# Optimization experiments

Hardware: AMD Instinct MI355X
Metric: run time of the kernel (lower is better)

Reference implementation:

```python
import jax, jax.numpy as jnp
import numpy as np

N, E, IC, H, OC, K = 100000, 1600000, 64, 64, 16, 4
BN_EPS = 1e-5


def setup_inputs() -> dict:
    key = jax.random.key(0)
    ks = jax.random.split(key, 32)
    s = 0.05
    inp = {
        'x': jax.random.normal(ks[0], (N, IC), jnp.float32),
        'edge_index': jax.random.randint(ks[1], (2, E), 0, N, jnp.int32),
        # ChebConv weights: K linear maps (no bias) + one bias per conv (PyG ChebConv)
        'W1': jax.random.normal(ks[2], (K, IC, H), jnp.float32) * s,
        'bc1': jax.random.normal(ks[3], (H,), jnp.float32) * s,
        'W2': jax.random.normal(ks[4], (K, H, H), jnp.float32) * s,
        'bc2': jax.random.normal(ks[5], (H,), jnp.float32) * s,
        'W3': jax.random.normal(ks[6], (K, H, H), jnp.float32) * s,
        'bc3': jax.random.normal(ks[7], (H,), jnp.float32) * s,
        # BatchNorm1d params + running stats (eval mode)
        'g1': 1.0 + 0.1 * jax.random.normal(ks[8], (H,), jnp.float32),
        'be1': 0.1 * jax.random.normal(ks[9], (H,), jnp.float32),
        'rm1': 0.1 * jax.random.normal(ks[10], (H,), jnp.float32),
        'rv1': jax.random.uniform(ks[11], (H,), jnp.float32, 0.5, 1.5),
        'g2': 1.0 + 0.1 * jax.random.normal(ks[12], (H,), jnp.float32),
        'be2': 0.1 * jax.random.normal(ks[13], (H,), jnp.float32),
        'rm2': 0.1 * jax.random.normal(ks[14], (H,), jnp.float32),
        'rv2': jax.random.uniform(ks[15], (H,), jnp.float32, 0.5, 1.5),
        'g3': 1.0 + 0.1 * jax.random.normal(ks[16], (H,), jnp.float32),
        'be3': 0.1 * jax.random.normal(ks[17], (H,), jnp.float32),
        'rm3': 0.1 * jax.random.normal(ks[18], (H,), jnp.float32),
        'rv3': jax.random.uniform(ks[19], (H,), jnp.float32, 0.5, 1.5),
        # head Linear(h, oc)
        'headW': jax.random.normal(ks[20], (H, OC), jnp.float32) * s,
        'headB': jax.random.normal(ks[21], (OC,), jnp.float32) * s,
    }
    return inp


def _prop(x, src, dst, w):
    # one sparse propagation: out[dst] += w_e * x[src]  (== L_hat @ x)
    return jax.ops.segment_sum(w[:, None] * x[src], dst, num_segments=N)


def _cheb(x, src, dst, w, W, b):
    # Chebyshev recursion: T0 = x, T1 = L_hat x, T_k = 2 L_hat T_{k-1} - T_{k-2}
    Tx0 = x
    out = Tx0 @ W[0]
    Tx1 = _prop(x, src, dst, w)
    out = out + Tx1 @ W[1]
    for k in range(2, W.shape[0]):
        Tx2 = 2.0 * _prop(Tx1, src, dst, w) - Tx0
        out = out + Tx2 @ W[k]
        Tx0, Tx1 = Tx1, Tx2
    return out + b


def _bn(x, g, b, rm, rv):
    # BatchNorm1d in eval mode: affine with running stats
    return (x - rm) * (g * jax.lax.rsqrt(rv + BN_EPS)) + b


def reference(x, edge_index, W1, bc1, W2, bc2, W3, bc3,
              g1, be1, rm1, rv1, g2, be2, rm2, rv2, g3, be3, rm3, rv3,
              headW, headB):
    src, dst = edge_index[0], edge_index[1]
    # sym-normalized scaled Laplacian (lambda_max=2): L_hat = -D^{-1/2} A D^{-1/2}
    deg = jax.ops.segment_sum(jnp.ones((E,), x.dtype), src, num_segments=N)
    dinv = jnp.where(deg > 0, jax.lax.rsqrt(jnp.maximum(deg, 1.0)), 0.0)
    w = -dinv[src] * dinv[dst]
    h = jax.nn.relu(_bn(_cheb(x, src, dst, w, W1, bc1), g1, be1, rm1, rv1))
    h = jax.nn.relu(_bn(_cheb(h, src, dst, w, W2, bc2), g2, be2, rm2, rv2))
    h = jax.nn.relu(_bn(_cheb(h, src, dst, w, W3, bc3), g3, be3, rm3, rv3))
    return h @ headW + headB
```

## Files before the change

### kernel.cpp

```cpp
#include <hip/hip_runtime.h>

#define NN 100000
#define EE 1600000
#define HD 64
#define OCD 16
#define NBUCK 391
#define CAP 5888
#define BN_EPS 1e-5f

typedef unsigned short u16;
typedef unsigned long long u64;
typedef __attribute__((ext_vector_type(8))) short short8v;
typedef __attribute__((ext_vector_type(4))) float f32x4;

union f32u32 { float f; unsigned int u; };

__device__ __forceinline__ float bflo(unsigned int u) {
    f32u32 c; c.u = u << 16; return c.f;
}
__device__ __forceinline__ float bfhi(unsigned int u) {
    f32u32 c; c.u = u & 0xffff0000u; return c.f;
}
__device__ __forceinline__ float bf2f(u16 u) {
    f32u32 c; c.u = (unsigned int)u << 16; return c.f;
}
__device__ __forceinline__ u16 f2bf(float f) {
    f32u32 c; c.f = f;
    unsigned int r = 0x7fffu + ((c.u >> 16) & 1u);
    return (u16)((c.u + r) >> 16);
}

__global__ __launch_bounds__(256) void bucketA_kernel(
        const int* __restrict__ src, const int* __restrict__ dst,
        int* __restrict__ gcd, u64* __restrict__ bregion) {
    __shared__ int lh[NBUCK], lbase[NBUCK], lcur[NBUCK];
    int t = threadIdx.x;
    int ebase = blockIdx.x * 4096;

    for (int i = t; i < NBUCK; i += 256) lh[i] = 0;
    __syncthreads();

    int es[16], ed[16];
    #pragma unroll
    for (int j = 0; j < 16; ++j) {
        int e = ebase + j * 256 + t;
        if (e < EE) {
            es[j] = src[e]; ed[j] = dst[e];
            atomicAdd(&lh[ed[j] >> 8], 1);
        } else { es[j] = -1; ed[j] = 0; }
    }
    __syncthreads();
    for (int i = t; i < NBUCK; i += 256) {
        int c = lh[i];
        lbase[i] = (c > 0) ? atomicAdd(&gcd[i * 16], c) : 0;
        lcur[i] = 0;
    }
    __syncthreads();
    #pragma unroll
    for (int j = 0; j < 16; ++j) {
        if (es[j] >= 0) {
            int b = ed[j] >> 8;
            int r = atomicAdd(&lcur[b], 1);
            int pos = lbase[b] + r;
            if (pos < CAP)
                bregion[(size_t)b * CAP + pos] =
                    (u64)(unsigned int)es[j] | ((u64)(unsigned int)ed[j] << 32);
        }
    }
}

__global__ __launch_bounds__(256) void bucketA2_kernel(
        const int* __restrict__ src,
        int* __restrict__ gcs, int* __restrict__ sregion) {
    __shared__ int lh[NBUCK], lbase[NBUCK], lcur[NBUCK];
    int t = threadIdx.x;
    int ebase = blockIdx.x * 4096;

    for (int i = t; i < NBUCK; i += 256) lh[i] = 0;
    __syncthreads();

    int es[16];
    #pragma unroll
    for (int j = 0; j < 16; ++j) {
        int e = ebase + j * 256 + t;
        if (e < EE) {
            es[j] = src[e];
            atomicAdd(&lh[es[j] >> 8], 1);
        } else es[j] = -1;
    }
    __syncthreads();
    for (int i = t; i < NBUCK; i += 256) {
        int c = lh[i];
        lbase[i] = (c > 0) ? atomicAdd(&gcs[i * 16], c) : 0;
        lcur[i] = 0;
    }
    __syncthreads();
    #pragma unroll
    for (int j = 0; j < 16; ++j) {
        if (es[j] >= 0) {
            int b = es[j] >> 8;
            int r = atomicAdd(&lcur[b], 1);
            int pos = lbase[b] + r;
            if (pos < CAP)
                sregion[(size_t)b * CAP + pos] = es[j];
        }
    }
}

__global__ __launch_bounds__(256) void bucketB_kernel(
        const int* __restrict__ gcd, const u64* __restrict__ bregion,
        int* __restrict__ rstart, int* __restrict__ deg,
        int* __restrict__ colp) {
    __shared__ int lh[256], lsc[256], lcur[256];
    int b = blockIdx.x, t = threadIdx.x;
    int cnt = min(gcd[b * 16], CAP - 768);
    size_t base = (size_t)b * CAP;

    lh[t] = 0;
    __syncthreads();
    for (int i = t; i < cnt; i += 256) {
        int d = (int)(bregion[base + i] >> 32);
        atomicAdd(&lh[d & 255], 1);
    }
    __syncthreads();
    int deg4 = (lh[t] + 3) & ~3;
    lsc[t] = deg4;
    __syncthreads();
    for (int o = 1; o < 256; o <<= 1) {
        int v = (t >= o) ? lsc[t - o] : 0;
        __syncthreads();
        lsc[t] += v;
        __syncthreads();
    }
    int excl = lsc[t] - deg4;
    int node = b * 256 + t;
    if (node < NN) {
        rstart[node] = (int)base + excl;
        deg[node] = lh[t];
    }
    lcur[t] = excl;
    __syncthreads();
    for (int i = t; i < cnt; i += 256) {
        u64 pair = bregion[base + i];
        int s = (int)(unsigned int)(pair & 0xffffffffu);
        int dl = ((int)(pair >> 32)) & 255;
        int p = atomicAdd(&lcur[dl], 1);
        colp[base + p] = s;
    }
}

__global__ __launch_bounds__(256) void bucketB2_kernel(
        const int* __restrict__ gcs, const int* __restrict__ sregion,
        int* __restrict__ cs) {
    __shared__ int lh[256];
    int b = blockIdx.x, t = threadIdx.x;
    int cnt = min(gcs[b * 16], CAP);
    size_t base = (size_t)b * CAP;

    lh[t] = 0;
    __syncthreads();
    for (int i = t; i < cnt; i += 256)
        atomicAdd(&lh[sregion[base + i] & 255], 1);
    __syncthreads();
    int node = b * 256 + t;
    if (node < NN) cs[node] = lh[t];
}

__global__ void dinv_kernel(const int* __restrict__ cs, float* __restrict__ dinv,
                            float* __restrict__ ndsq, float* __restrict__ sdeg) {
    int i = blockIdx.x * 256 + threadIdx.x;
    if (i < NN) {
        int d = cs[i];
        float di = (d > 0) ? rsqrtf((float)d) : 0.0f;
        dinv[i] = di;
        ndsq[i] = -di * di;
        sdeg[i] = (d > 0) ? sqrtf((float)d) : 0.0f;
    }
}

__global__ void fold_kernel(const float* __restrict__ W, const float* __restrict__ bc,
                            const float* __restrict__ g, const float* __restrict__ be,
                            const float* __restrict__ rm, const float* __restrict__ rv,
                            u16* __restrict__ Wfrag, float* __restrict__ biasf) {
    int idx = blockIdx.x * 256 + threadIdx.x;
    if (idx >= 16384) return;
    int km = idx >> 12, r = idx & 4095, i = r >> 6, h = r & 63;
    float sc = g[h] * rsqrtf(rv[h] + BN_EPS);
    int e = i * 64 + h;
    float wv;
    if      (km == 0) wv = (W[e] - W[8192 + e]) * sc;
    else if (km == 1) wv = (W[4096 + e] - 3.0f * W[12288 + e]) * sc;
    else if (km == 2) wv = 2.0f * W[8192 + e] * sc;
    else              wv = 4.0f * W[12288 + e] * sc;
    u16 hi = f2bf(wv);
    u16 lo = f2bf(wv - bf2f(hi));
    int lane = (((i & 31) >> 3) << 4) | (h & 15);
    int base = (km * 2) * 4096 + (i >> 5) * 2048 + (h >> 4) * 512 + lane * 8 + (i & 7);
    Wfrag[base] = hi;
    Wfrag[base + 4096] = lo;
    if (idx < 64)
        biasf[idx] = (bc[idx] - rm[idx]) * g[idx] * rsqrtf(rv[idx] + BN_EPS) + be[idx];
}

__global__ void scale0_kernel(const float* __restrict__ x, const float* __restrict__ dinv,
                              u16* __restrict__ Xhi, u16* __restrict__ Xlo,
                              u16* __restrict__ P0) {
    int idx = blockIdx.x * 256 + threadIdx.x;
    if (idx >= NN * (HD / 4)) return;
    int n = idx >> 4;
    float di = dinv[n];
    float4 v = ((const float4*)x)[idx];
    float vv[4] = {v.x, v.y, v.z, v.w};
    u16 hi[4], lo[4], p[4];
    #pragma unroll
    for (int j = 0; j < 4; ++j) {
        hi[j] = f2bf(vv[j]);
        lo[j] = f2bf(vv[j] - bf2f(hi[j]));
        p[j]  = f2bf(di * vv[j]);
    }
    *(u64*)(&Xhi[(size_t)idx * 4]) = *(u64*)hi;
    *(u64*)(&Xlo[(size_t)idx * 4]) = *(u64*)lo;
    *(u64*)(&P0 [(size_t)idx * 4]) = *(u64*)p;
}

__global__ __launch_bounds__(256) void prop_kernel(
        const u16* __restrict__ Pin, u16* __restrict__ Pout,
        const int* __restrict__ rstart, const int* __restrict__ deg,
        const int* __restrict__ col, const float* __restrict__ ndsq) {
    int d = blockIdx.x * 4 + (threadIdx.x >> 6);
    if (d >= NN) return;
    int lane = threadIdx.x & 63;
    int g = lane >> 4;
    int l = lane & 15;
    int e0 = rstart[d], e1 = e0 + deg[d];

    float a0 = 0.f, a1 = 0.f, a2 = 0.f, a3 = 0.f;
    for (int c = e0 + g * 4; c < e1; c += 16) {
        if (c + 4 <= e1) {
            int4 c4 = *(const int4*)(col + c);
            uint2 u0 = *(const uint2*)(Pin + (size_t)c4.x * HD + l * 4);
            uint2 u1 = *(const uint2*)(Pin + (size_t)c4.y * HD + l * 4);
            uint2 u2 = *(const uint2*)(Pin + (size_t)c4.z * HD + l * 4);
            uint2 u3 = *(const uint2*)(Pin + (size_t)c4.w * HD + l * 4);
            a0 += bflo(u0.x); a1 += bfhi(u0.x); a2 += bflo(u0.y); a3 += bfhi(u0.y);
            a0 += bflo(u1.x); a1 += bfhi(u1.x); a2 += bflo(u1.y); a3 += bfhi(u1.y);
            a0 += bflo(u2.x); a1 += bfhi(u2.x); a2 += bflo(u2.y); a3 += bfhi(u2.y);
            a0 += bflo(u3.x); a1 += bfhi(u3.x); a2 += bflo(u3.y); a3 += bfhi(u3.y);
        } else {
            for (int j = 0; j < e1 - c; ++j) {
                int s = col[c + j];
                uint2 u = *(const uint2*)(Pin + (size_t)s * HD + l * 4);
                a0 += bflo(u.x); a1 += bfhi(u.x);
                a2 += bflo(u.y); a3 += bfhi(u.y);
            }
        }
    }
    a0 += __shfl_xor(a0, 16); a1 += __shfl_xor(a1, 16);
    a2 += __shfl_xor(a2, 16); a3 += __shfl_xor(a3, 16);
    a0 += __shfl_xor(a0, 32); a1 += __shfl_xor(a1, 32);
    a2 += __shfl_xor(a2, 32); a3 += __shfl_xor(a3, 32);

    if (g == 0) {
        float nd = ndsq[d];
        uint2 o;
        o.x = (unsigned int)f2bf(nd * a0) | ((unsigned int)f2bf(nd * a1) << 16);
        o.y = (unsigned int)f2bf(nd * a2) | ((unsigned int)f2bf(nd * a3) << 16);
        *(uint2*)(Pout + (size_t)d * HD + l * 4) = o;
    }
}

template<bool FUSE_HEAD>
__global__ __launch_bounds__(256) void combine_kernel(
        const u16* __restrict__ Xhi, const u16* __restrict__ Xlo,
        const u16* __restrict__ P1, const u16* __restrict__ P2,
        const u16* __restrict__ P3,
        const float* __restrict__ sdeg, const float* __restrict__ dinv,
        const u16* __restrict__ Wfrag, const float* __restrict__ biasf,
        u16* __restrict__ outDhi, u16* __restrict__ outDlo, u16* __restrict__ outP0,
        const float* __restrict__ headW, const float* __restrict__ headB,
        float* __restrict__ out16) {
    int t = threadIdx.x;
    int w = t >> 6;
    int l = t & 63;
    int nbase = blockIdx.x * 64;

    int arow = nbase + w * 16 + (l & 15);
    if (arow > NN - 1) arow = NN - 1;
    size_t abase = (size_t)arow * HD;

    f32x4 accX[4], accP[4];
    #pragma unroll
    for (int nt = 0; nt < 4; ++nt) {
        accX[nt] = (f32x4){0.f, 0.f, 0.f, 0.f};
        accP[nt] = (f32x4){0.f, 0.f, 0.f, 0.f};
    }

    #pragma unroll
    for (int ks = 0; ks < 2; ++ks) {
        size_t ao = abase + ks * 32 + (l >> 4) * 8;
        short8v aXhi = *(const short8v*)(Xhi + ao);
        short8v aXlo = *(const short8v*)(Xlo + ao);
        short8v aP1  = *(const short8v*)(P1  + ao);
        short8v aP2  = *(const short8v*)(P2  + ao);
        short8v aP3  = *(const short8v*)(P3  + ao);
        #pragma unroll
        for (int nt = 0; nt < 4; ++nt) {
            const u16* wb = Wfrag + ks * 2048 + nt * 512 + l * 8;
            short8v b0h = *(const short8v*)(wb);
            short8v b0l = *(const short8v*)(wb + 4096);
            short8v b1h = *(const short8v*)(wb + 8192);
            short8v b1l = *(const short8v*)(wb + 12288);
            short8v b2h = *(const short8v*)(wb + 16384);
            short8v b2l = *(const short8v*)(wb + 20480);
            short8v b3h = *(const short8v*)(wb + 24576);
            short8v b3l = *(const short8v*)(wb + 28672);
            accX[nt] = __builtin_amdgcn_mfma_f32_16x16x32_bf16(aXhi, b0h, accX[nt], 0, 0, 0);
            accX[nt] = __builtin_amdgcn_mfma_f32_16x16x32_bf16(aXlo, b0h, accX[nt], 0, 0, 0);
            accX[nt] = __builtin_amdgcn_mfma_f32_16x16x32_bf16(aXhi, b0l, accX[nt], 0, 0, 0);
            accP[nt] = __builtin_amdgcn_mfma_f32_16x16x32_bf16(aP1,  b1h, accP[nt], 0, 0, 0);
            accP[nt] = __builtin_amdgcn_mfma_f32_16x16x32_bf16(aP1,  b1l, accP[nt], 0, 0, 0);
            accP[nt] = __builtin_amdgcn_mfma_f32_16x16x32_bf16(aP2,  b2h, accP[nt], 0, 0, 0);
            accP[nt] = __builtin_amdgcn_mfma_f32_16x16x32_bf16(aP2,  b2l, accP[nt], 0, 0, 0);
            accP[nt] = __builtin_amdgcn_mfma_f32_16x16x32_bf16(aP3,  b3h, accP[nt], 0, 0, 0);
            accP[nt] = __builtin_amdgcn_mfma_f32_16x16x32_bf16(aP3,  b3l, accP[nt], 0, 0, 0);
        }
    }

    int col = l & 15;
    int rbase = w * 16 + (l >> 4) * 4;

    if (!FUSE_HEAD) {
        #pragma unroll
        for (int nt = 0; nt < 4; ++nt) {
            int h = nt * 16 + col;
            float bi = biasf[h];
            #pragma unroll
            for (int reg = 0; reg < 4; ++reg) {
                int node = nbase + rbase + reg;
                int nodeL = node > NN - 1 ? NN - 1 : node;
                float val = accX[nt][reg] + sdeg[nodeL] * accP[nt][reg] + bi;
                val = fmaxf(val, 0.f);
                if (node < NN) {
                    u16 hi = f2bf(val);
                    size_t o = (size_t)node * HD + h;
                    outDhi[o] = hi;
                    outDlo[o] = f2bf(val - bf2f(hi));
                    outP0[o]  = f2bf(dinv[nodeL] * val);
                }
            }
        }
    } else {
        __shared__ float Tl[64][68];
        __shared__ float Wl[HD * OCD];
        #pragma unroll
        for (int nt = 0; nt < 4; ++nt) {
            int h = nt * 16 + col;
            float bi = biasf[h];
            #pragma unroll
            for (int reg = 0; reg < 4; ++reg) {
                int node = nbase + rbase + reg;
                int nodeL = node > NN - 1 ? NN - 1 : node;
                float val = accX[nt][reg] + sdeg[nodeL] * accP[nt][reg] + bi;
                Tl[rbase + reg][h] = fmaxf(val, 0.f);
            }
        }
        ((float4*)Wl)[t & 255] = ((const float4*)headW)[t & 255];
        __syncthreads();

        int n = t >> 2;
        int oc0 = (t & 3) * 4;
        float4 o;
        o.x = headB[oc0]; o.y = headB[oc0 + 1]; o.z = headB[oc0 + 2]; o.w = headB[oc0 + 3];
        #pragma unroll 8
        for (int i = 0; i < 64; ++i) {
            float tv = Tl[n][i];
            const float* wr = &Wl[i * OCD + oc0];
            o.x = fmaf(tv, wr[0], o.x);
            o.y = fmaf(tv, wr[1], o.y);
            o.z = fmaf(tv, wr[2], o.z);
            o.w = fmaf(tv, wr[3], o.w);
        }
        int nn = nbase + n;
        if (nn < NN) *(float4*)(&out16[(size_t)nn * OCD + oc0]) = o;
    }
}

static inline size_t al256(size_t x) { return (x + 255) & ~(size_t)255; }

extern "C" void kernel_launch(void* const* d_in, const int* in_sizes, int n_in,
                              void* d_out, int out_size, void* d_ws, size_t ws_size,
                              hipStream_t stream) {
    const float* x     = (const float*)d_in[0];
    const int*   ei    = (const int*)  d_in[1];
    const float* W1    = (const float*)d_in[2];
    const float* bc1   = (const float*)d_in[3];
    const float* W2    = (const float*)d_in[4];
    const float* bc2   = (const float*)d_in[5];
    const float* W3    = (const float*)d_in[6];
    const float* bc3   = (const float*)d_in[7];
    const float* g1  = (const float*)d_in[8],  *be1 = (const float*)d_in[9];
    const float* rm1 = (const float*)d_in[10], *rv1 = (const float*)d_in[11];
    const float* g2  = (const float*)d_in[12], *be2 = (const float*)d_in[13];
    const float* rm2 = (const float*)d_in[14], *rv2 = (const float*)d_in[15];
    const float* g3  = (const float*)d_in[16], *be3 = (const float*)d_in[17];
    const float* rm3 = (const float*)d_in[18], *rv3 = (const float*)d_in[19];
    const float* headW = (const float*)d_in[20];
    const float* headB = (const float*)d_in[21];

    const int* src = ei;
    const int* dst = ei + EE;

    char* w = (char*)d_ws;
    size_t off = 0;
    auto take = [&](size_t bytes) { char* p = w + off; off += al256(bytes); return p; };
    float* dinv   = (float*)take(NN * 4);
    float* ndsq   = (float*)take(NN * 4);
    float* sdeg   = (float*)take(NN * 4);
    int*   cs     = (int*)  take(NN * 4);
    int*   deg    = (int*)  take(NN * 4);
    int*   rstart = (int*)  take(NN * 4);
    int*   gc     = (int*)  take(2 * NBUCK * 16 * 4);
    int*   gcd    = gc;
    int*   gcs    = gc + NBUCK * 16;
    u64*   bregion= (u64*)  take((size_t)NBUCK * CAP * 8);
    int*   sregion= (int*)  take((size_t)NBUCK * CAP * 4);
    int*   colp   = (int*)  take((size_t)NBUCK * CAP * 4);
    u16*   Wfrag1 = (u16*)  take(32768 * 2);
    u16*   Wfrag2 = (u16*)  take(32768 * 2);
    u16*   Wfrag3 = (u16*)  take(32768 * 2);
    float* bf1    = (float*)take(64 * 4);
    float* bf2    = (float*)take(64 * 4);
    float* bf3    = (float*)take(64 * 4);
    const size_t NH = (size_t)NN * HD;
    u16* Xhi = (u16*)take(NH * 2);
    u16* Xlo = (u16*)take(NH * 2);
    u16* Yhi = (u16*)take(NH * 2);
    u16* Ylo = (u16*)take(NH * 2);
    u16* P0  = (u16*)take(NH * 2);
    u16* P1  = (u16*)take(NH * 2);
    u16* P2  = (u16*)take(NH * 2);
    u16* P3  = (u16*)take(NH * 2);

    const int AB = (EE + 4095) / 4096;
    const int NG = (NN + 255) / 256;
    const int PROP_GRID = (NN + 3) / 4;
    const int CB_GRID   = (NN + 63) / 64;
    const int S0_GRID   = (NN * (HD / 4) + 255) / 256;

    hipMemsetAsync(gc, 0, 2 * NBUCK * 16 * 4, stream);
    bucketA_kernel <<<AB, 256, 0, stream>>>(src, dst, gcd, bregion);
    bucketA2_kernel<<<AB, 256, 0, stream>>>(src, gcs, sregion);
    bucketB_kernel <<<NBUCK, 256, 0, stream>>>(gcd, bregion, rstart, deg, colp);
    bucketB2_kernel<<<NBUCK, 256, 0, stream>>>(gcs, sregion, cs);
    dinv_kernel<<<NG, 256, 0, stream>>>(cs, dinv, ndsq, sdeg);
    fold_kernel<<<64, 256, 0, stream>>>(W1, bc1, g1, be1, rm1, rv1, Wfrag1, bf1);
    fold_kernel<<<64, 256, 0, stream>>>(W2, bc2, g2, be2, rm2, rv2, Wfrag2, bf2);
    fold_kernel<<<64, 256, 0, stream>>>(W3, bc3, g3, be3, rm3, rv3, Wfrag3, bf3);
    scale0_kernel<<<S0_GRID, 256, 0, stream>>>(x, dinv, Xhi, Xlo, P0);

    float* out16 = (float*)d_out;

    prop_kernel<<<PROP_GRID, 256, 0, stream>>>(P0, P1, rstart, deg, colp, ndsq);
    prop_kernel<<<PROP_GRID, 256, 0, stream>>>(P1, P2, rstart, deg, colp, ndsq);
    prop_kernel<<<PROP_GRID, 256, 0, stream>>>(P2, P3, rstart, deg, colp, ndsq);
    combine_kernel<false><<<CB_GRID, 256, 0, stream>>>(
        Xhi, Xlo, P1, P2, P3, sdeg, dinv, Wfrag1, bf1,
        Yhi, Ylo, P0, nullptr, nullptr, nullptr);
    prop_kernel<<<PROP_GRID, 256, 0, stream>>>(P0, P1, rstart, deg, colp, ndsq);
    prop_kernel<<<PROP_GRID, 256, 0, stream>>>(P1, P2, rstart, deg, colp, ndsq);
    prop_kernel<<<PROP_GRID, 256, 0, stream>>>(P2, P3, rstart, deg, colp, ndsq);
    combine_kernel<false><<<CB_GRID, 256, 0, stream>>>(
        Yhi, Ylo, P1, P2, P3, sdeg, dinv, Wfrag2, bf2,
        Xhi, Xlo, P0, nullptr, nullptr, nullptr);
    prop_kernel<<<PROP_GRID, 256, 0, stream>>>(P0, P1, rstart, deg, colp, ndsq);
    prop_kernel<<<PROP_GRID, 256, 0, stream>>>(P1, P2, rstart, deg, colp, ndsq);
    prop_kernel<<<PROP_GRID, 256, 0, stream>>>(P2, P3, rstart, deg, colp, ndsq);
    combine_kernel<true><<<CB_GRID, 256, 0, stream>>>(
        Xhi, Xlo, P1, P2, P3, sdeg, dinv, Wfrag3, bf3,
        nullptr, nullptr, nullptr, headW, headB, out16);
}
```

Measured before the change: 675.6 us.

## Split propagation feature vectors into four 16-wide slabs for cache locality

Stores the P buffers as four column slabs of 16 bf16 features per node, so each slab (NN*16*2 bytes, about 3.2MB) fits better in cache during gathers. The prop kernel now runs one block per slab and node-quad, with 16 edges processed in parallel per wave, each touching 32 bytes. The combine and scale kernels are updated to read and write the slab layout. The cost is four times as many prop blocks, more reads of the column index list, and narrower gather transactions.

Result: slower. 1.256 ms (+86.0%).

```diff
diff --git a/kernel.cpp b/kernel.cpp
--- a/kernel.cpp
+++ b/kernel.cpp
@@ -206,66 +206,66 @@
                               u16* __restrict__ Xhi, u16* __restrict__ Xlo,
                               u16* __restrict__ P0) {
     int idx = blockIdx.x * 256 + threadIdx.x;
-    if (idx >= NN * (HD / 4)) return;
-    int n = idx >> 4;
+    if (idx >= 4 * NN) return;
+    int s = idx / NN, n = idx - s * NN;
     float di = dinv[n];
-    float4 v = ((const float4*)x)[idx];
-    float vv[4] = {v.x, v.y, v.z, v.w};
-    u16 hi[4], lo[4], p[4];
-    #pragma unroll
-    for (int j = 0; j < 4; ++j) {
-        hi[j] = f2bf(vv[j]);
-        lo[j] = f2bf(vv[j] - bf2f(hi[j]));
-        p[j]  = f2bf(di * vv[j]);
-    }
-    *(u64*)(&Xhi[(size_t)idx * 4]) = *(u64*)hi;
-    *(u64*)(&Xlo[(size_t)idx * 4]) = *(u64*)lo;
-    *(u64*)(&P0 [(size_t)idx * 4]) = *(u64*)p;
+    const float4* xr = (const float4*)(x + (size_t)n * HD + s * 16);
+    u16 hi[16], lo[16], p[16];
+    #pragma unroll
+    for (int q = 0; q < 4; ++q) {
+        float4 v = xr[q];
+        float vv[4] = {v.x, v.y, v.z, v.w};
+        #pragma unroll
+        for (int j = 0; j < 4; ++j) {
+            int f = q * 4 + j;
+            hi[f] = f2bf(vv[j]);
+            lo[f] = f2bf(vv[j] - bf2f(hi[f]));
+            p[f]  = f2bf(di * vv[j]);
+        }
+    }
+    uint4* xh = (uint4*)(Xhi + (size_t)n * HD + s * 16);
+    uint4* xl = (uint4*)(Xlo + (size_t)n * HD + s * 16);
+    uint4* pp = (uint4*)(P0 + ((size_t)s * NN + n) * 16);
+    xh[0] = ((const uint4*)hi)[0]; xh[1] = ((const uint4*)hi)[1];
+    xl[0] = ((const uint4*)lo)[0]; xl[1] = ((const uint4*)lo)[1];
+    pp[0] = ((const uint4*)p)[0];  pp[1] = ((const uint4*)p)[1];
 }
 
 __global__ __launch_bounds__(256) void prop_kernel(
         const u16* __restrict__ Pin, u16* __restrict__ Pout,
         const int* __restrict__ rstart, const int* __restrict__ deg,
         const int* __restrict__ col, const float* __restrict__ ndsq) {
-    int d = blockIdx.x * 4 + (threadIdx.x >> 6);
+    int bid = blockIdx.x;
+    int s = bid & 3;
+    int d = (bid >> 2) * 4 + (threadIdx.x >> 6);
     if (d >= NN) return;
     int lane = threadIdx.x & 63;
-    int g = lane >> 4;
-    int l = lane & 15;
+    int g = lane >> 2;
+    int l = lane & 3;
+    const u16* Ps = Pin + (size_t)s * NN * 16;
+    u16* Pd = Pout + (size_t)s * NN * 16;
     int e0 = rstart[d], e1 = e0 + deg[d];
 
     float a0 = 0.f, a1 = 0.f, a2 = 0.f, a3 = 0.f;
-    for (int c = e0 + g * 4; c < e1; c += 16) {
-        if (c + 4 <= e1) {
-            int4 c4 = *(const int4*)(col + c);
-            uint2 u0 = *(const uint2*)(Pin + (size_t)c4.x * HD + l * 4);
-            uint2 u1 = *(const uint2*)(Pin + (size_t)c4.y * HD + l * 4);
-            uint2 u2 = *(const uint2*)(Pin + (size_t)c4.z * HD + l * 4);
-            uint2 u3 = *(const uint2*)(Pin + (size_t)c4.w * HD + l * 4);
-            a0 += bflo(u0.x); a1 += bfhi(u0.x); a2 += bflo(u0.y); a3 += bfhi(u0.y);
-            a0 += bflo(u1.x); a1 += bfhi(u1.x); a2 += bflo(u1.y); a3 += bfhi(u1.y);
-            a0 += bflo(u2.x); a1 += bfhi(u2.x); a2 += bflo(u2.y); a3 += bfhi(u2.y);
-            a0 += bflo(u3.x); a1 += bfhi(u3.x); a2 += bflo(u3.y); a3 += bfhi(u3.y);
-        } else {
-            for (int j = 0; j < e1 - c; ++j) {
-                int s = col[c + j];
-                uint2 u = *(const uint2*)(Pin + (size_t)s * HD + l * 4);
-                a0 += bflo(u.x); a1 += bfhi(u.x);
-                a2 += bflo(u.y); a3 += bfhi(u.y);
-            }
-        }
-    }
-    a0 += __shfl_xor(a0, 16); a1 += __shfl_xor(a1, 16);
-    a2 += __shfl_xor(a2, 16); a3 += __shfl_xor(a3, 16);
-    a0 += __shfl_xor(a0, 32); a1 += __shfl_xor(a1, 32);
-    a2 += __shfl_xor(a2, 32); a3 += __shfl_xor(a3, 32);
-
+    for (int e = e0 + g; e < e1; e += 16) {
+        int sc = col[e];
+        uint2 u = *(const uint2*)(Ps + (size_t)sc * 16 + l * 4);
+        a0 += bflo(u.x); a1 += bfhi(u.x);
+        a2 += bflo(u.y); a3 += bfhi(u.y);
+    }
+    #pragma unroll
+    for (int m = 4; m <= 32; m <<= 1) {
+        a0 += __shfl_xor(a0, m);
+        a1 += __shfl_xor(a1, m);
+        a2 += __shfl_xor(a2, m);
+        a3 += __shfl_xor(a3, m);
+    }
     if (g == 0) {
         float nd = ndsq[d];
         uint2 o;
         o.x = (unsigned int)f2bf(nd * a0) | ((unsigned int)f2bf(nd * a1) << 16);
         o.y = (unsigned int)f2bf(nd * a2) | ((unsigned int)f2bf(nd * a3) << 16);
-        *(uint2*)(Pout + (size_t)d * HD + l * 4) = o;
+        *(uint2*)(Pd + (size_t)d * 16 + l * 4) = o;
     }
 }
 
@@ -297,12 +297,14 @@
 
     #pragma unroll
     for (int ks = 0; ks < 2; ++ks) {
-        size_t ao = abase + ks * 32 + (l >> 4) * 8;
+        int fb = ks * 32 + (l >> 4) * 8;
+        size_t ao = abase + fb;
+        size_t po = ((size_t)(fb >> 4) * NN + arow) * 16 + (fb & 15);
         short8v aXhi = *(const short8v*)(Xhi + ao);
         short8v aXlo = *(const short8v*)(Xlo + ao);
-        short8v aP1  = *(const short8v*)(P1  + ao);
-        short8v aP2  = *(const short8v*)(P2  + ao);
-        short8v aP3  = *(const short8v*)(P3  + ao);
+        short8v aP1  = *(const short8v*)(P1 + po);
+        short8v aP2  = *(const short8v*)(P2 + po);
+        short8v aP3  = *(const short8v*)(P3 + po);
         #pragma unroll
         for (int nt = 0; nt < 4; ++nt) {
             const u16* wb = Wfrag + ks * 2048 + nt * 512 + l * 8;
@@ -345,7 +347,7 @@
                     size_t o = (size_t)node * HD + h;
                     outDhi[o] = hi;
                     outDlo[o] = f2bf(val - bf2f(hi));
-                    outP0[o]  = f2bf(dinv[nodeL] * val);
+                    outP0[((size_t)nt * NN + node) * 16 + col] = f2bf(dinv[nodeL] * val);
                 }
             }
         }
@@ -443,9 +445,9 @@
 
     const int AB = (EE + 4095) / 4096;
     const int NG = (NN + 255) / 256;
-    const int PROP_GRID = (NN + 3) / 4;
+    const int PROP_GRID = 4 * ((NN + 3) / 4);
     const int CB_GRID   = (NN + 63) / 64;
-    const int S0_GRID   = (NN * (HD / 4) + 255) / 256;
+    const int S0_GRID   = (4 * NN + 255) / 256;
 
     hipMemsetAsync(gc, 0, 2 * NBUCK * 16 * 4, stream);
     bucketA_kernel <<<AB, 256, 0, stream>>>(src, dst, gcd, bregion);
```
